# Kernel tuning notes

Measured on AMD Instinct MI355X. Metric: run time of the kernel, lower is better.

The kernel has to match this reference:

```python
import jax, jax.numpy as jnp
import numpy as np

N = 50000
E = 800000
IN_DIM = 128
HID = 256
NCLASS = 40
ORDER = 3
LOCAL_NOISE = 0.5


def setup_inputs() -> dict:
    key = jax.random.key(0)
    ks = jax.random.split(key, 8)
    feats = jax.random.normal(ks[0], (N, IN_DIM), dtype=jnp.float32)
    edge_row = jax.random.randint(ks[1], (E,), 0, N, dtype=jnp.int32)
    edge_col = jax.random.randint(ks[2], (E,), 0, N, dtype=jnp.int32)
    edge_vals = jax.random.uniform(ks[3], (E,), dtype=jnp.float32) / 16.0  # ~row-normalized adjacency
    W1 = jax.random.normal(ks[4], (IN_DIM, HID), dtype=jnp.float32) * (1.0 / np.sqrt(IN_DIM))
    b1 = jnp.zeros((HID,), dtype=jnp.float32)
    W2 = jax.random.normal(ks[5], (HID, NCLASS), dtype=jnp.float32) * (1.0 / np.sqrt(HID))
    b2 = jnp.zeros((NCLASS,), dtype=jnp.float32)
    return {"feats": feats, "edge_row": edge_row, "edge_col": edge_col,
            "edge_vals": edge_vals, "W1": W1, "b1": b1, "W2": W2, "b2": b2}


def _spmm(edge_row, edge_col, edge_vals, x):
    # y[r] = sum_e vals[e] * x[col[e]] for edges with row[e]==r
    msgs = edge_vals[:, None] * x[edge_col]  # [E, D]
    return jax.ops.segment_sum(msgs, edge_row, num_segments=N)


def reference(feats, edge_row, edge_col, edge_vals, W1, b1, W2, b2):
    # eval path: drop_node scales by (1 - drop_rate)
    x = feats * (1.0 - LOCAL_NOISE)
    # GRANDConv_NX: K-hop propagation with running-sum average
    y = x
    h = x
    for _ in range(ORDER):
        h = _spmm(edge_row, edge_col, edge_vals, h)
        y = y + h
    feat = y / (ORDER + 1.0)
    # MLP (use_bn=False, dropout inactive at eval)
    h1 = jax.nn.relu(feat @ W1 + b1)
    logits = h1 @ W2 + b2
    # MLP.forward applies log_softmax, outer forward applies it again
    out = jax.nn.log_softmax(jax.nn.log_softmax(logits, axis=-1), axis=-1)
    return out
```

## Files before the change

kernel.cpp:

```cpp
#include <hip/hip_runtime.h>
#include <math.h>

#define N_NODES 50000
#define N_EDGES 800000
#define IN_DIM 128
#define HID 256
#define NCLASS 40

#define SCAN_NBLK 49

#define HBLK 256
#define EPB  3125
#define PK   12500

typedef __attribute__((ext_vector_type(8))) short short8;
typedef __attribute__((ext_vector_type(4))) float floatx4;

__device__ inline unsigned bf16pair(float a, float b) {
    unsigned ua = __float_as_uint(a), ub = __float_as_uint(b);
    ua = (ua + 0x7fffu + ((ua >> 16) & 1u)) >> 16;
    ub = (ub + 0x7fffu + ((ub >> 16) & 1u)) >> 16;
    return ua | (ub << 16);
}
__device__ inline unsigned bf16bits(float a) {
    unsigned ua = __float_as_uint(a);
    return (ua + 0x7fffu + ((ua >> 16) & 1u)) >> 16;
}
__device__ inline float bf_lo(unsigned u) { return __uint_as_float(u << 16); }
__device__ inline float bf_hi(unsigned u) { return __uint_as_float(u & 0xffff0000u); }

__global__ void prep_kernel(const float4* __restrict__ f4,
                            uint2* __restrict__ fb16,
                            const float* __restrict__ W1,
                            uint4* __restrict__ W1frag) {
    int i = blockIdx.x * blockDim.x + threadIdx.x;
    float4 v = f4[i];
    fb16[i] = make_uint2(bf16pair(v.x, v.y), bf16pair(v.z, v.w));
    if (i < 4096) {
        int f = i;
        int h = f >> 11, rem = f & 2047;
        int t = rem >> 8, s = (rem >> 6) & 3, l = rem & 63;
        int q = l >> 4, n16 = l & 15;
        int n = h * 128 + t * 16 + n16;
        int kb = s * 32 + q * 8;
        unsigned p[4];
        #pragma unroll
        for (int jj = 0; jj < 4; ++jj) {
            float a = W1[(size_t)(kb + 2 * jj) * HID + n];
            float b = W1[(size_t)(kb + 2 * jj + 1) * HID + n];
            p[jj] = bf16pair(a, b);
        }
        W1frag[f] = make_uint4(p[0], p[1], p[2], p[3]);
    }
}

__global__ __launch_bounds__(1024) void hist_kernel(const int* __restrict__ rows,
                                                    unsigned* __restrict__ hist) {
    __shared__ unsigned h[PK];
    int t = threadIdx.x;
    for (int i = t; i < PK / 4; i += 1024)
        ((uint4*)h)[i] = make_uint4(0u, 0u, 0u, 0u);
    __syncthreads();
    int e0 = blockIdx.x * EPB;
    for (int i = t; i < EPB; i += 1024) {
        int r = rows[e0 + i];
        atomicAdd(&h[r >> 2], 1u << ((r & 3) * 8));
    }
    __syncthreads();
    unsigned* out = hist + (size_t)blockIdx.x * PK;
    for (int i = t; i < PK / 4; i += 1024)
        ((uint4*)out)[i] = ((const uint4*)h)[i];
}

__global__ void colscan_kernel(const unsigned* __restrict__ hist,
                               unsigned* __restrict__ base,
                               int* __restrict__ counts,
                               int* __restrict__ blockSums) {
    int t = blockIdx.x * 256 + threadIdx.x;
    unsigned run = 0;
    if (t < PK) {
        #pragma unroll 8
        for (int b = 0; b < HBLK; ++b) {
            unsigned v = hist[b * PK + t];
            base[b * PK + t] = run;
            run += v;
        }
        *(int4*)(counts + 4 * t) = make_int4((int)(run & 0xffu), (int)((run >> 8) & 0xffu),
                                             (int)((run >> 16) & 0xffu), (int)(run >> 24));
    }
    int s = (int)((run & 0xffu) + ((run >> 8) & 0xffu) + ((run >> 16) & 0xffu) + (run >> 24));
    #pragma unroll
    for (int off = 32; off >= 1; off >>= 1)
        s += __shfl_xor(s, off);
    __shared__ int wsum[4];
    int lane = threadIdx.x & 63, wid = threadIdx.x >> 6;
    if (lane == 0) wsum[wid] = s;
    __syncthreads();
    if (threadIdx.x == 0)
        blockSums[blockIdx.x] = wsum[0] + wsum[1] + wsum[2] + wsum[3];
}

__global__ void block_offset_kernel(const int* __restrict__ blockSums,
                                    int* __restrict__ blockOffs,
                                    int* __restrict__ row_start) {
    int lane = threadIdx.x;
    int x = (lane < SCAN_NBLK) ? blockSums[lane] : 0;
    #pragma unroll
    for (int off = 1; off < 64; off <<= 1) {
        int y = __shfl_up(x, off);
        if (lane >= off) x += y;
    }
    int excl = __shfl_up(x, 1);
    if (lane == 0) excl = 0;
    if (lane < SCAN_NBLK) blockOffs[lane] = excl;
    if (lane == SCAN_NBLK - 1) row_start[N_NODES] = x;
}

__global__ void local_scan_kernel(const int* __restrict__ counts,
                                  const int* __restrict__ blockOffs,
                                  int* __restrict__ row_start) {
    int t = threadIdx.x;
    int base = blockIdx.x * 1024 + t * 4;
    int4 c = make_int4(0, 0, 0, 0);
    if (base < N_NODES) c = *(const int4*)(counts + base);
    int s0 = c.x, s1 = s0 + c.y, s2 = s1 + c.z, s3 = s2 + c.w;
    int tsum = s3;
    int lane = t & 63, wid = t >> 6;
    int x = tsum;
    #pragma unroll
    for (int off = 1; off < 64; off <<= 1) {
        int y = __shfl_up(x, off);
        if (lane >= off) x += y;
    }
    __shared__ int wsum[4];
    if (lane == 63) wsum[wid] = x;
    __syncthreads();
    int woff = 0;
    for (int i = 0; i < 4; ++i)
        if (i < wid) woff += wsum[i];
    int excl = x - tsum + woff + blockOffs[blockIdx.x];
    if (base < N_NODES) {
        int4 rs = make_int4(excl, excl + s0, excl + s1, excl + s2);
        *(int4*)(row_start + base) = rs;
    }
}

__global__ __launch_bounds__(1024) void scatter2_kernel(const int* __restrict__ rows,
                                                        const int* __restrict__ cols,
                                                        const float* __restrict__ vals,
                                                        const unsigned* __restrict__ base,
                                                        const int* __restrict__ row_start,
                                                        unsigned* __restrict__ csr_cv) {
    __shared__ unsigned cur[PK];
    int t = threadIdx.x;
    const uint4* bb = (const uint4*)(base + (size_t)blockIdx.x * PK);
    for (int i = t; i < PK / 4; i += 1024)
        ((uint4*)cur)[i] = bb[i];
    __syncthreads();
    int e0 = blockIdx.x * EPB;
    for (int i = t; i < EPB; i += 1024) {
        int e = e0 + i;
        int r = rows[e];
        unsigned sh = (unsigned)(r & 3) * 8u;
        unsigned old = atomicAdd(&cur[r >> 2], 1u << sh);
        int pos = row_start[r] + (int)((old >> sh) & 0xffu);
        csr_cv[pos] = ((unsigned)cols[e] << 16) | bf16bits(vals[e]);
    }
}

template <int MODE>
__global__ void spmm_csr(const int* __restrict__ row_start,
                         const unsigned* __restrict__ csr_cv,
                         const uint4* __restrict__ Hin4,
                         uint4* __restrict__ Hout4,
                         const float* __restrict__ feats,
                         const uint4* __restrict__ h1b4,
                         const uint4* __restrict__ h2b4) {
    int wave = (blockIdx.x * blockDim.x + threadIdx.x) >> 6;
    int lane = threadIdx.x & 63;
    if (wave >= N_NODES) return;
    int p = lane >> 4;
    int q = lane & 15;
    int start = row_start[wave];
    int end   = row_start[wave + 1];
    float acc[8] = {};
    for (int base = start; base < end; base += 64) {
        int idx = base + lane;
        unsigned u = 0;
        if (idx < end) u = csr_cv[idx];
        int cnt = min(64, end - base);
        for (int j = 0; j < cnt; j += 8) {
            unsigned uj0 = __shfl(u, j + p);
            unsigned uj1 = __shfl(u, j + 4 + p);
            int   c0 = uj0 >> 16;
            int   c1 = uj1 >> 16;
            float v0 = __uint_as_float(uj0 << 16);
            float v1 = __uint_as_float(uj1 << 16);
            uint4 h0 = Hin4[(size_t)c0 * 16 + q];
            uint4 h1 = Hin4[(size_t)c1 * 16 + q];
            acc[0] += v0 * bf_lo(h0.x);
            acc[1] += v0 * bf_hi(h0.x);
            acc[2] += v0 * bf_lo(h0.y);
            acc[3] += v0 * bf_hi(h0.y);
            acc[4] += v0 * bf_lo(h0.z);
            acc[5] += v0 * bf_hi(h0.z);
            acc[6] += v0 * bf_lo(h0.w);
            acc[7] += v0 * bf_hi(h0.w);
            acc[0] += v1 * bf_lo(h1.x);
            acc[1] += v1 * bf_hi(h1.x);
            acc[2] += v1 * bf_lo(h1.y);
            acc[3] += v1 * bf_hi(h1.y);
            acc[4] += v1 * bf_lo(h1.z);
            acc[5] += v1 * bf_hi(h1.z);
            acc[6] += v1 * bf_lo(h1.w);
            acc[7] += v1 * bf_hi(h1.w);
        }
    }
    #pragma unroll
    for (int i = 0; i < 8; ++i) {
        acc[i] += __shfl_xor(acc[i], 16);
        acc[i] += __shfl_xor(acc[i], 32);
    }
    if (p == 0) {
        size_t o16 = (size_t)wave * 16 + q;
        if (MODE == 1) {
            #pragma unroll
            for (int i = 0; i < 8; ++i) acc[i] *= 0.5f;
        } else if (MODE == 2) {
            size_t of = (size_t)wave * IN_DIM + q * 8;
            float4 f0 = *(const float4*)(feats + of);
            float4 f1 = *(const float4*)(feats + of + 4);
            uint4 a = h1b4[o16];
            uint4 b = h2b4[o16];
            acc[0] += 0.5f * f0.x + bf_lo(a.x) + bf_lo(b.x);
            acc[1] += 0.5f * f0.y + bf_hi(a.x) + bf_hi(b.x);
            acc[2] += 0.5f * f0.z + bf_lo(a.y) + bf_lo(b.y);
            acc[3] += 0.5f * f0.w + bf_hi(a.y) + bf_hi(b.y);
            acc[4] += 0.5f * f1.x + bf_lo(a.z) + bf_lo(b.z);
            acc[5] += 0.5f * f1.y + bf_hi(a.z) + bf_hi(b.z);
            acc[6] += 0.5f * f1.z + bf_lo(a.w) + bf_lo(b.w);
            acc[7] += 0.5f * f1.w + bf_hi(a.w) + bf_hi(b.w);
        }
        Hout4[o16] = make_uint4(bf16pair(acc[0], acc[1]), bf16pair(acc[2], acc[3]),
                                bf16pair(acc[4], acc[5]), bf16pair(acc[6], acc[7]));
    }
}

__global__ void gemm1_mfma(const uint4* __restrict__ yb4,
                           const uint4* __restrict__ W1frag,
                           const float* __restrict__ bias1,
                           float* __restrict__ H1) {
    __shared__ uint4 wlds[2048];
    int tid = threadIdx.x;
    int h = blockIdx.y;
    for (int i = tid; i < 2048; i += 256)
        wlds[i] = W1frag[h * 2048 + i];
    __syncthreads();

    int wave = tid >> 6, lane = tid & 63;
    int q = lane >> 4, c16 = lane & 15;
    int row0 = blockIdx.x * 64 + wave * 16;
    int arow = row0 + c16;

    union { uint4 u; short8 v; } au[4], bu;
    if (arow < N_NODES) {
        #pragma unroll
        for (int s = 0; s < 4; ++s)
            au[s].u = yb4[(size_t)arow * 16 + 4 * s + q];
    } else {
        #pragma unroll
        for (int s = 0; s < 4; ++s)
            au[s].u = make_uint4(0u, 0u, 0u, 0u);
    }

    #pragma unroll
    for (int t = 0; t < 8; ++t) {
        floatx4 acc = {0.f, 0.f, 0.f, 0.f};
        #pragma unroll
        for (int s = 0; s < 4; ++s) {
            bu.u = wlds[(t * 4 + s) * 64 + lane];
            acc = __builtin_amdgcn_mfma_f32_16x16x32_bf16(au[s].v, bu.v, acc, 0, 0, 0);
        }
        int col = h * 128 + t * 16 + c16;
        float bs = bias1[col];
        #pragma unroll
        for (int r = 0; r < 4; ++r) {
            int crow = row0 + q * 4 + r;
            if (crow < N_NODES) {
                float v = 0.25f * acc[r] + bs;
                H1[(size_t)crow * HID + col] = v > 0.f ? v : 0.f;
            }
        }
    }
}

#define G2_BM 128
#define G2_BK 32
__global__ void gemm2_kernel(const float* __restrict__ H1,
                             const float* __restrict__ W2,
                             float* __restrict__ part0,
                             float* __restrict__ part1) {
    __shared__ float As[G2_BK][G2_BM + 4];
    __shared__ float Bs[G2_BK][44];
    int tid = threadIdx.x;
    int rt = tid >> 3;
    int ct = tid & 7;
    int row0 = blockIdx.x * G2_BM;
    int kbase = blockIdx.y * (HID / 2);
    float* outp = blockIdx.y ? part1 : part0;
    float acc[4][5] = {};
    for (int kt = 0; kt < HID / 2; kt += G2_BK) {
        int k0 = kbase + kt;
        #pragma unroll
        for (int i = tid; i < 1024; i += 256) {
            int r = i >> 3, u = i & 7;
            int gr = row0 + r;
            float4 v = make_float4(0.f, 0.f, 0.f, 0.f);
            if (gr < N_NODES)
                v = *(const float4*)(H1 + (size_t)gr * HID + k0 + u * 4);
            int kb = u * 4;
            As[kb + 0][r] = v.x;
            As[kb + 1][r] = v.y;
            As[kb + 2][r] = v.z;
            As[kb + 3][r] = v.w;
        }
        for (int i = tid; i < 320; i += 256) {
            int r = i / 10, cg = i % 10;
            float4 w = *(const float4*)(W2 + (size_t)(k0 + r) * NCLASS + cg * 4);
            *(float4*)&Bs[r][cg * 4] = w;
        }
        __syncthreads();
        #pragma unroll
        for (int kk = 0; kk < G2_BK; ++kk) {
            float4 a0 = *(const float4*)&As[kk][rt * 4];
            float a[4] = {a0.x, a0.y, a0.z, a0.w};
            float b[5];
            #pragma unroll
            for (int j = 0; j < 5; ++j) b[j] = Bs[kk][ct * 5 + j];
            #pragma unroll
            for (int i = 0; i < 4; ++i)
                #pragma unroll
                for (int j = 0; j < 5; ++j)
                    acc[i][j] += a[i] * b[j];
        }
        __syncthreads();
    }
    #pragma unroll
    for (int i = 0; i < 4; ++i) {
        int gr = row0 + rt * 4 + i;
        if (gr >= N_NODES) continue;
        float* dst = outp + (size_t)gr * NCLASS + ct * 5;
        #pragma unroll
        for (int j = 0; j < 5; ++j)
            dst[j] = acc[i][j];
    }
}

__global__ void lsm_kernel(const float* __restrict__ part0,
                           const float* __restrict__ part1,
                           const float* __restrict__ b2,
                           float* __restrict__ Out) {
    int wave = threadIdx.x >> 6;
    int lane = threadIdx.x & 63;
    int row = blockIdx.x * 4 + wave;
    if (row >= N_NODES) return;

    float acc = -INFINITY;
    if (lane < NCLASS) {
        size_t idx = (size_t)row * NCLASS + lane;
        acc = part0[idx] + part1[idx] + b2[lane];
    }

    float m = acc;
    #pragma unroll
    for (int off = 32; off >= 1; off >>= 1)
        m = fmaxf(m, __shfl_xor(m, off));
    float ex = (lane < NCLASS) ? expf(acc - m) : 0.f;
    float s = ex;
    #pragma unroll
    for (int off = 32; off >= 1; off >>= 1)
        s += __shfl_xor(s, off);
    float z1 = acc - (m + logf(s));

    float m2 = z1;
    #pragma unroll
    for (int off = 32; off >= 1; off >>= 1)
        m2 = fmaxf(m2, __shfl_xor(m2, off));
    float ex2 = (lane < NCLASS) ? expf(z1 - m2) : 0.f;
    float s2 = ex2;
    #pragma unroll
    for (int off = 32; off >= 1; off >>= 1)
        s2 += __shfl_xor(s2, off);
    float z2 = z1 - (m2 + logf(s2));

    if (lane < NCLASS)
        Out[(size_t)row * NCLASS + lane] = z2;
}

extern "C" void kernel_launch(void* const* d_in, const int* in_sizes, int n_in,
                              void* d_out, int out_size, void* d_ws, size_t ws_size,
                              hipStream_t stream) {
    const float* feats   = (const float*)d_in[0];
    const int*   e_row   = (const int*)d_in[1];
    const int*   e_col   = (const int*)d_in[2];
    const float* e_vals  = (const float*)d_in[3];
    const float* W1      = (const float*)d_in[4];
    const float* b1      = (const float*)d_in[5];
    const float* W2      = (const float*)d_in[6];
    const float* b2      = (const float*)d_in[7];
    float* out = (float*)d_out;

    float* ws    = (float*)d_ws;
    uint4* ybf4  = (uint4*)ws;
    unsigned* hist = (unsigned*)ws;
    uint4* W1frag = (uint4*)(ws + (size_t)N_NODES * IN_DIM / 2);
    int*   counts = (int*)(ws + 3300000);
    uint4* fb16_4 = (uint4*)(ws + (size_t)N_NODES * IN_DIM);
    uint4* h1b4  = (uint4*)(ws + (size_t)N_NODES * IN_DIM * 3 / 2);
    uint4* h2b4  = (uint4*)(ws + (size_t)N_NODES * IN_DIM * 2);
    unsigned* basep = (unsigned*)(ws + (size_t)N_NODES * IN_DIM * 5 / 2);
    float* hid   = ws + (size_t)N_NODES * IN_DIM;
    float* part0 = ws;
    float* part1 = ws + (size_t)N_NODES * NCLASS;

    unsigned* csr_cv = (unsigned*)d_out;
    int*   row_start = (int*)d_out + 2 * N_EDGES;
    int*   blockSums = row_start + N_NODES + 4;
    int*   blockOffs = blockSums + 64;

    const int ELEMS4 = N_NODES * IN_DIM / 4;
    prep_kernel<<<ELEMS4 / 256, 256, 0, stream>>>((const float4*)feats, (uint2*)fb16_4,
                                                  W1, W1frag);

    hist_kernel<<<HBLK, 1024, 0, stream>>>(e_row, hist);
    colscan_kernel<<<SCAN_NBLK, 256, 0, stream>>>(hist, basep, counts, blockSums);
    block_offset_kernel<<<1, 64, 0, stream>>>(blockSums, blockOffs, row_start);
    local_scan_kernel<<<SCAN_NBLK, 256, 0, stream>>>(counts, blockOffs, row_start);
    scatter2_kernel<<<HBLK, 1024, 0, stream>>>(e_row, e_col, e_vals, basep,
                                               row_start, csr_cv);

    const int SPMM_BLOCKS = N_NODES / 4;
    spmm_csr<1><<<SPMM_BLOCKS, 256, 0, stream>>>(row_start, csr_cv, fb16_4, h1b4,
                                                 nullptr, nullptr, nullptr);
    spmm_csr<0><<<SPMM_BLOCKS, 256, 0, stream>>>(row_start, csr_cv, h1b4, h2b4,
                                                 nullptr, nullptr, nullptr);
    spmm_csr<2><<<SPMM_BLOCKS, 256, 0, stream>>>(row_start, csr_cv, h2b4, ybf4,
                                                 feats, h1b4, h2b4);

    dim3 g1((N_NODES + 63) / 64, 2);
    gemm1_mfma<<<g1, 256, 0, stream>>>(ybf4, W1frag, b1, hid);

    dim3 g2((N_NODES + G2_BM - 1) / G2_BM, 2);
    gemm2_kernel<<<g2, 256, 0, stream>>>(hid, W2, part0, part1);

    lsm_kernel<<<(N_NODES + 3) / 4, 256, 0, stream>>>(part0, part1, b2, out);
}
```

Before: 278.0 us.

## Split SpMM feature dimension across grid.y and fold block-offset scan into local scan

The SpMM kernel now splits the 128-wide bf16 feature row into four 32-column slices, one per grid.y block. Each wave handles 8 edges at a time with 8-byte loads per lane, instead of 4 edges with 16-byte loads. This multiplies the number of waves, aiming at better latency hiding and occupancy for the gather-bound propagation, at the cost of re-reading CSR indices four times. Nontemporal loads and stores are added for streamed data. The separate single-wave block_offset kernel is removed, with each local_scan block computing the block-sum prefix itself, which saves one launch.

```diff
diff --git a/kernel.cpp b/kernel.cpp
--- a/kernel.cpp
+++ b/kernel.cpp
@@ -15,6 +15,7 @@
 
 typedef __attribute__((ext_vector_type(8))) short short8;
 typedef __attribute__((ext_vector_type(4))) float floatx4;
+typedef __attribute__((ext_vector_type(2))) unsigned uintx2;
 
 __device__ inline unsigned bf16pair(float a, float b) {
     unsigned ua = __float_as_uint(a), ub = __float_as_uint(b);
@@ -100,26 +101,25 @@
         blockSums[blockIdx.x] = wsum[0] + wsum[1] + wsum[2] + wsum[3];
 }
 
-__global__ void block_offset_kernel(const int* __restrict__ blockSums,
-                                    int* __restrict__ blockOffs,
-                                    int* __restrict__ row_start) {
-    int lane = threadIdx.x;
-    int x = (lane < SCAN_NBLK) ? blockSums[lane] : 0;
-    #pragma unroll
-    for (int off = 1; off < 64; off <<= 1) {
-        int y = __shfl_up(x, off);
-        if (lane >= off) x += y;
-    }
-    int excl = __shfl_up(x, 1);
-    if (lane == 0) excl = 0;
-    if (lane < SCAN_NBLK) blockOffs[lane] = excl;
-    if (lane == SCAN_NBLK - 1) row_start[N_NODES] = x;
-}
-
 __global__ void local_scan_kernel(const int* __restrict__ counts,
-                                  const int* __restrict__ blockOffs,
+                                  const int* __restrict__ blockSums,
                                   int* __restrict__ row_start) {
+    __shared__ int wsum[4];
+    __shared__ int boff;
     int t = threadIdx.x;
+    if (t < 64) {
+        int x = (t < SCAN_NBLK) ? blockSums[t] : 0;
+        #pragma unroll
+        for (int off = 1; off < 64; off <<= 1) {
+            int y = __shfl_up(x, off);
+            if (t >= off) x += y;
+        }
+        int excl = __shfl_up(x, 1);
+        if (t == 0) excl = 0;
+        if (t == blockIdx.x) boff = excl;
+        if (blockIdx.x == SCAN_NBLK - 1 && t == SCAN_NBLK - 1)
+            row_start[N_NODES] = x;
+    }
     int base = blockIdx.x * 1024 + t * 4;
     int4 c = make_int4(0, 0, 0, 0);
     if (base < N_NODES) c = *(const int4*)(counts + base);
@@ -132,13 +132,12 @@
         int y = __shfl_up(x, off);
         if (lane >= off) x += y;
     }
-    __shared__ int wsum[4];
     if (lane == 63) wsum[wid] = x;
     __syncthreads();
     int woff = 0;
     for (int i = 0; i < 4; ++i)
         if (i < wid) woff += wsum[i];
-    int excl = x - tsum + woff + blockOffs[blockIdx.x];
+    int excl = x - tsum + woff + boff;
     if (base < N_NODES) {
         int4 rs = make_int4(excl, excl + s0, excl + s1, excl + s2);
         *(int4*)(row_start + base) = rs;
@@ -171,78 +170,60 @@
 template <int MODE>
 __global__ void spmm_csr(const int* __restrict__ row_start,
                          const unsigned* __restrict__ csr_cv,
-                         const uint4* __restrict__ Hin4,
-                         uint4* __restrict__ Hout4,
+                         const uintx2* __restrict__ Hin2,
+                         uintx2* __restrict__ Hout2,
                          const float* __restrict__ feats,
-                         const uint4* __restrict__ h1b4,
-                         const uint4* __restrict__ h2b4) {
-    int wave = (blockIdx.x * blockDim.x + threadIdx.x) >> 6;
+                         const uintx2* __restrict__ h1b2,
+                         const uintx2* __restrict__ h2b2) {
+    int row  = blockIdx.x * 4 + (threadIdx.x >> 6);
     int lane = threadIdx.x & 63;
-    if (wave >= N_NODES) return;
-    int p = lane >> 4;
-    int q = lane & 15;
-    int start = row_start[wave];
-    int end   = row_start[wave + 1];
-    float acc[8] = {};
+    int s    = blockIdx.y;
+    int p = lane >> 3;
+    int q = lane & 7;
+    int start = row_start[row];
+    int end   = row_start[row + 1];
+    float a0 = 0.f, a1 = 0.f, a2 = 0.f, a3 = 0.f;
     for (int base = start; base < end; base += 64) {
         int idx = base + lane;
         unsigned u = 0;
-        if (idx < end) u = csr_cv[idx];
+        if (idx < end) u = __builtin_nontemporal_load(csr_cv + idx);
         int cnt = min(64, end - base);
         for (int j = 0; j < cnt; j += 8) {
-            unsigned uj0 = __shfl(u, j + p);
-            unsigned uj1 = __shfl(u, j + 4 + p);
-            int   c0 = uj0 >> 16;
-            int   c1 = uj1 >> 16;
-            float v0 = __uint_as_float(uj0 << 16);
-            float v1 = __uint_as_float(uj1 << 16);
-            uint4 h0 = Hin4[(size_t)c0 * 16 + q];
-            uint4 h1 = Hin4[(size_t)c1 * 16 + q];
-            acc[0] += v0 * bf_lo(h0.x);
-            acc[1] += v0 * bf_hi(h0.x);
-            acc[2] += v0 * bf_lo(h0.y);
-            acc[3] += v0 * bf_hi(h0.y);
-            acc[4] += v0 * bf_lo(h0.z);
-            acc[5] += v0 * bf_hi(h0.z);
-            acc[6] += v0 * bf_lo(h0.w);
-            acc[7] += v0 * bf_hi(h0.w);
-            acc[0] += v1 * bf_lo(h1.x);
-            acc[1] += v1 * bf_hi(h1.x);
-            acc[2] += v1 * bf_lo(h1.y);
-            acc[3] += v1 * bf_hi(h1.y);
-            acc[4] += v1 * bf_lo(h1.z);
-            acc[5] += v1 * bf_hi(h1.z);
-            acc[6] += v1 * bf_lo(h1.w);
-            acc[7] += v1 * bf_hi(h1.w);
-        }
-    }
-    #pragma unroll
-    for (int i = 0; i < 8; ++i) {
-        acc[i] += __shfl_xor(acc[i], 16);
-        acc[i] += __shfl_xor(acc[i], 32);
+            unsigned uj = __shfl(u, j + p);
+            int   c = uj >> 16;
+            float v = __uint_as_float(uj << 16);
+            uintx2 h = Hin2[(size_t)c * 32 + s * 8 + q];
+            a0 += v * bf_lo(h.x);
+            a1 += v * bf_hi(h.x);
+            a2 += v * bf_lo(h.y);
+            a3 += v * bf_hi(h.y);
+        }
+    }
+    #pragma unroll
+    for (int off = 8; off <= 32; off <<= 1) {
+        a0 += __shfl_xor(a0, off);
+        a1 += __shfl_xor(a1, off);
+        a2 += __shfl_xor(a2, off);
+        a3 += __shfl_xor(a3, off);
     }
     if (p == 0) {
-        size_t o16 = (size_t)wave * 16 + q;
+        size_t o = (size_t)row * 32 + s * 8 + q;
         if (MODE == 1) {
-            #pragma unroll
-            for (int i = 0; i < 8; ++i) acc[i] *= 0.5f;
+            a0 *= 0.5f; a1 *= 0.5f; a2 *= 0.5f; a3 *= 0.5f;
         } else if (MODE == 2) {
-            size_t of = (size_t)wave * IN_DIM + q * 8;
-            float4 f0 = *(const float4*)(feats + of);
-            float4 f1 = *(const float4*)(feats + of + 4);
-            uint4 a = h1b4[o16];
-            uint4 b = h2b4[o16];
-            acc[0] += 0.5f * f0.x + bf_lo(a.x) + bf_lo(b.x);
-            acc[1] += 0.5f * f0.y + bf_hi(a.x) + bf_hi(b.x);
-            acc[2] += 0.5f * f0.z + bf_lo(a.y) + bf_lo(b.y);
-            acc[3] += 0.5f * f0.w + bf_hi(a.y) + bf_hi(b.y);
-            acc[4] += 0.5f * f1.x + bf_lo(a.z) + bf_lo(b.z);
-            acc[5] += 0.5f * f1.y + bf_hi(a.z) + bf_hi(b.z);
-            acc[6] += 0.5f * f1.z + bf_lo(a.w) + bf_lo(b.w);
-            acc[7] += 0.5f * f1.w + bf_hi(a.w) + bf_hi(b.w);
-        }
-        Hout4[o16] = make_uint4(bf16pair(acc[0], acc[1]), bf16pair(acc[2], acc[3]),
-                                bf16pair(acc[4], acc[5]), bf16pair(acc[6], acc[7]));
+            size_t of = (size_t)row * IN_DIM + s * 32 + q * 4;
+            floatx4 f = __builtin_nontemporal_load((const floatx4*)(feats + of));
+            uintx2 A = __builtin_nontemporal_load(h1b2 + o);
+            uintx2 B = __builtin_nontemporal_load(h2b2 + o);
+            a0 += 0.5f * f.x + bf_lo(A.x) + bf_lo(B.x);
+            a1 += 0.5f * f.y + bf_hi(A.x) + bf_hi(B.x);
+            a2 += 0.5f * f.z + bf_lo(A.y) + bf_lo(B.y);
+            a3 += 0.5f * f.w + bf_hi(A.y) + bf_hi(B.y);
+        }
+        uintx2 r;
+        r.x = bf16pair(a0, a1);
+        r.y = bf16pair(a2, a3);
+        __builtin_nontemporal_store(r, Hout2 + o);
     }
 }
 
@@ -426,7 +407,6 @@
     unsigned* csr_cv = (unsigned*)d_out;
     int*   row_start = (int*)d_out + 2 * N_EDGES;
     int*   blockSums = row_start + N_NODES + 4;
-    int*   blockOffs = blockSums + 64;
 
     const int ELEMS4 = N_NODES * IN_DIM / 4;
     prep_kernel<<<ELEMS4 / 256, 256, 0, stream>>>((const float4*)feats, (uint2*)fb16_4,
@@ -434,18 +414,18 @@
 
     hist_kernel<<<HBLK, 1024, 0, stream>>>(e_row, hist);
     colscan_kernel<<<SCAN_NBLK, 256, 0, stream>>>(hist, basep, counts, blockSums);
-    block_offset_kernel<<<1, 64, 0, stream>>>(blockSums, blockOffs, row_start);
-    local_scan_kernel<<<SCAN_NBLK, 256, 0, stream>>>(counts, blockOffs, row_start);
+    local_scan_kernel<<<SCAN_NBLK, 256, 0, stream>>>(counts, blockSums, row_start);
     scatter2_kernel<<<HBLK, 1024, 0, stream>>>(e_row, e_col, e_vals, basep,
                                                row_start, csr_cv);
 
-    const int SPMM_BLOCKS = N_NODES / 4;
-    spmm_csr<1><<<SPMM_BLOCKS, 256, 0, stream>>>(row_start, csr_cv, fb16_4, h1b4,
-                                                 nullptr, nullptr, nullptr);
-    spmm_csr<0><<<SPMM_BLOCKS, 256, 0, stream>>>(row_start, csr_cv, h1b4, h2b4,
-                                                 nullptr, nullptr, nullptr);
-    spmm_csr<2><<<SPMM_BLOCKS, 256, 0, stream>>>(row_start, csr_cv, h2b4, ybf4,
-                                                 feats, h1b4, h2b4);
+    dim3 spg(N_NODES / 4, 4);
+    spmm_csr<1><<<spg, 256, 0, stream>>>(row_start, csr_cv, (const uintx2*)fb16_4,
+                                         (uintx2*)h1b4, nullptr, nullptr, nullptr);
+    spmm_csr<0><<<spg, 256, 0, stream>>>(row_start, csr_cv, (const uintx2*)h1b4,
+                                         (uintx2*)h2b4, nullptr, nullptr, nullptr);
+    spmm_csr<2><<<spg, 256, 0, stream>>>(row_start, csr_cv, (const uintx2*)h2b4,
+                                         (uintx2*)ybf4, feats,
+                                         (const uintx2*)h1b4, (const uintx2*)h2b4);
 
     dim3 g1((N_NODES + 63) / 64, 2);
     gemm1_mfma<<<g1, 256, 0, stream>>>(ybf4, W1frag, b1, hid);
```

Result: slower. 417.4 us (+50.1%).
